# Performance work log

Hardware: AMD Instinct MI355X
Metric: run time of the kernel (lower is better)

Reference implementation:

```python
import jax, jax.numpy as jnp
import numpy as np

EMBED_DIM = 1024
NUM_HEADS = 16
SEQ = 2048
BATCH = 2


def setup_inputs() -> dict:
    key = jax.random.key(0)
    ks = jax.random.split(key, 9)
    E = EMBED_DIM
    gain = 1.0 / np.sqrt(2.0)  # xavier_uniform with gain 1/sqrt(2) (qkv_same_dim)
    limit = gain * np.sqrt(6.0 / (E + E))
    q = jax.random.normal(ks[0], (SEQ, BATCH, E), dtype=jnp.float32)
    k = jax.random.normal(ks[1], (SEQ, BATCH, E), dtype=jnp.float32)
    v = jax.random.normal(ks[2], (SEQ, BATCH, E), dtype=jnp.float32)
    Wq = jax.random.uniform(ks[3], (E, E), jnp.float32, -limit, limit)
    Wk = jax.random.uniform(ks[4], (E, E), jnp.float32, -limit, limit)
    Wv = jax.random.uniform(ks[5], (E, E), jnp.float32, -limit, limit)
    bq = jnp.zeros((E,), jnp.float32)
    bk = jnp.zeros((E,), jnp.float32)
    bv = jnp.zeros((E,), jnp.float32)
    return {"query": q, "key": k, "value": v,
            "Wq": Wq, "bq": bq, "Wk": Wk, "bk": bk, "Wv": Wv, "bv": bv}


def reference(query, key, value, Wq, bq, Wk, bk, Wv, bv):
    # Base Taylor attention path (norm_taylor=True, do_scale=True, has_out=False).
    L, B, E = query.shape
    H = NUM_HEADS
    hd = E // H
    scaling = E ** (-0.5)  # self.scaling = dim**-0.5, dim == embed_dim

    q = (query @ Wq + bq) * scaling          # (L, B, E)
    k = key @ Wk + bk                         # (S, B, E)
    v = value @ Wv + bv                       # (S, B, E)

    def split_heads(x):
        # (T, B, E) -> (B*H, T, hd)
        T = x.shape[0]
        return x.reshape(T, B * H, hd).transpose(1, 0, 2)

    qh, kh, vh = split_heads(q), split_heads(k), split_heads(v)

    # Taylor expansion of exp(qk) to first order: 1 + q.k
    attn = 1.0 + jnp.einsum('bld,bsd->bls', qh, kh)   # (B*H, L, S)
    attn = attn / attn.sum(axis=-1, keepdims=True)    # row-normalize
    out = jnp.einsum('bls,bsd->bld', attn, vh)        # (B*H, L, hd)
    out = out.transpose(1, 0, 2).reshape(L, B, E)     # (L, B, E)
    return out
```

## Files before the change

kernel.cpp:

```cpp
#include <hip/hip_runtime.h>
#include <hip/hip_bf16.h>

#define L_SEQ 2048
#define BATCH 2
#define ROWS 4096
#define E 1024
#define NH 16
#define HD 64

typedef __attribute__((ext_vector_type(4))) float f32x4;
typedef __attribute__((ext_vector_type(8))) __bf16 bf16x8;

#define SWZ(byt) ((byt) ^ ((((byt) >> 7) & 7) << 4))

__device__ __forceinline__ void gload16(const void* g, void* l) {
    __builtin_amdgcn_global_load_lds((const __attribute__((address_space(1))) void*)g,
                                     (__attribute__((address_space(3))) void*)l,
                                     16, 0, 0);
}

__global__ __launch_bounds__(256) void convert_x(const float* __restrict__ q,
                                                 const float* __restrict__ k,
                                                 const float* __restrict__ v,
                                                 __bf16* __restrict__ Xb) {
    const int z = blockIdx.y;
    const float* src = (z == 0) ? q : ((z == 1) ? k : v);
    __bf16* dst = Xb + (size_t)z * ROWS * E;
    const size_t i = ((size_t)blockIdx.x * 256 + threadIdx.x) * 8;
    const float4 a = *(const float4*)(src + i);
    const float4 b = *(const float4*)(src + i + 4);
    bf16x8 o;
    o[0] = (__bf16)a.x; o[1] = (__bf16)a.y; o[2] = (__bf16)a.z; o[3] = (__bf16)a.w;
    o[4] = (__bf16)b.x; o[5] = (__bf16)b.y; o[6] = (__bf16)b.z; o[7] = (__bf16)b.w;
    *(bf16x8*)(dst + i) = o;
}

__global__ __launch_bounds__(256) void transpose_w(const float* __restrict__ Wq,
                                                   const float* __restrict__ Wk,
                                                   const float* __restrict__ Wv,
                                                   __bf16* __restrict__ Wt) {
    const int z = blockIdx.z;
    const float* W = (z == 0) ? Wq : ((z == 1) ? Wk : Wv);
    __bf16* dst = Wt + (size_t)z * E * E;
    __shared__ __align__(16) float t[64][65];
    const int n0 = blockIdx.x * 64, k0 = blockIdx.y * 64;
    const int r = threadIdx.x >> 2, c4 = threadIdx.x & 3;
#pragma unroll
    for (int j = 0; j < 4; ++j) {
        const float4 vv = *(const float4*)&W[(size_t)(k0 + r) * E + n0 + c4 * 16 + j * 4];
        t[r][c4 * 16 + j * 4 + 0] = vv.x;
        t[r][c4 * 16 + j * 4 + 1] = vv.y;
        t[r][c4 * 16 + j * 4 + 2] = vv.z;
        t[r][c4 * 16 + j * 4 + 3] = vv.w;
    }
    __syncthreads();
    bf16x8 o0, o1;
#pragma unroll
    for (int j = 0; j < 8; ++j) {
        o0[j] = (__bf16)t[c4 * 16 + j][r];
        o1[j] = (__bf16)t[c4 * 16 + 8 + j][r];
    }
    *(bf16x8*)&dst[(size_t)(n0 + r) * E + k0 + c4 * 16] = o0;
    *(bf16x8*)&dst[(size_t)(n0 + r) * E + k0 + c4 * 16 + 8] = o1;
}

__device__ __forceinline__ void stage_ht(const __bf16* __restrict__ gsrc, int row0, int kcol,
                                         char* ldsdst, int wv, int ln) {
#pragma unroll
    for (int r = 0; r < 2; ++r) {
        const int rowg = row0 + r * 64 + wv * 8 + (ln >> 3);
        const int c16 = (ln & 7) ^ (ln >> 3);
        gload16(gsrc + (size_t)rowg * E + kcol + c16 * 8,
                ldsdst + r * 8192 + wv * 1024);
    }
}

__device__ __forceinline__ bf16x8 fragld(const char* base, int row, int kk, int kg) {
    return *(const bf16x8*)(base + row * 128 + ((((kk << 2) | kg) ^ (row & 7)) << 4));
}

#define PH_SYNC_BEGIN  __builtin_amdgcn_s_barrier(); \
                       asm volatile("s_waitcnt lgkmcnt(0)" ::: "memory"); \
                       __builtin_amdgcn_sched_barrier(0); \
                       __builtin_amdgcn_s_setprio(1);
#define PH_SYNC_END    __builtin_amdgcn_s_setprio(0); \
                       __builtin_amdgcn_s_barrier();

__global__ __launch_bounds__(512, 2) void gemm_qkv(const __bf16* __restrict__ Xb,
                                                   const __bf16* __restrict__ Wt,
                                                   const float* __restrict__ bq,
                                                   const float* __restrict__ bk,
                                                   const float* __restrict__ bv,
                                                   __bf16* __restrict__ Cb) {
    extern __shared__ __align__(16) char smem[];
    const int z = blockIdx.z;
    const __bf16* A = Xb + (size_t)z * ROWS * E;
    const __bf16* B = Wt + (size_t)z * E * E;
    __bf16* C = Cb + (size_t)z * ROWS * E;
    const float* bias = (z == 0) ? bq : ((z == 1) ? bk : bv);
    const float alpha = (z == 0) ? 0.03125f : 1.0f;
    const int m0 = blockIdx.y * 256, n0 = blockIdx.x * 256;
    const int tid = threadIdx.x, ln = tid & 63, wv = tid >> 6;
    const int lr = ln & 15, kg = ln >> 4;
    const int wm = (wv & 3) * 64, wn = (wv >> 2) * 128;
    char* LA0 = smem;            char* LA1 = smem + 32768;
    char* LB0 = smem + 65536;    char* LB1 = smem + 98304;

    stage_ht(A, m0 + 0,   0,  LA0 + 0,     wv, ln);
    stage_ht(A, m0 + 128, 0,  LA0 + 16384, wv, ln);
    stage_ht(B, n0 + 0,   0,  LB0 + 0,     wv, ln);
    stage_ht(B, n0 + 128, 0,  LB0 + 16384, wv, ln);
    stage_ht(A, m0 + 0,   64, LA1 + 0,     wv, ln);
    stage_ht(A, m0 + 128, 64, LA1 + 16384, wv, ln);
    asm volatile("s_waitcnt vmcnt(4)" ::: "memory");
    __builtin_amdgcn_s_barrier();

    f32x4 acc[4][8] = {};
    bf16x8 Af[4][2], Bf[2][2];

#define LOAD_B(nb) \
    _Pragma("unroll") for (int nn = 0; nn < 2; ++nn) \
    _Pragma("unroll") for (int kk = 0; kk < 2; ++kk) \
        Bf[nn][kk] = fragld(cB, wn + ((nb) + nn) * 16 + lr, kk, kg);
#define QUAD(q) \
    _Pragma("unroll") for (int m = 0; m < 4; ++m) \
    _Pragma("unroll") for (int nn = 0; nn < 2; ++nn) \
    _Pragma("unroll") for (int kk = 0; kk < 2; ++kk) \
        acc[m][2 * (q) + nn] = __builtin_amdgcn_mfma_f32_16x16x32_bf16(Af[m][kk], Bf[nn][kk], acc[m][2 * (q) + nn], 0, 0, 0);

    for (int T = 0; T < 16; ++T) {
        const char* cA = (T & 1) ? LA1 : LA0;
        const char* cB = (T & 1) ? LB1 : LB0;
        char* nB = (T & 1) ? LB0 : LB1;
        char* nA = (T & 1) ? LA1 : LA0;
#pragma unroll
        for (int m = 0; m < 4; ++m)
#pragma unroll
            for (int kk = 0; kk < 2; ++kk)
                Af[m][kk] = fragld(cA, wm + m * 16 + lr, kk, kg);
        LOAD_B(0);
        if (T < 15) stage_ht(B, n0 + 0, (T + 1) * 64, nB + 0, wv, ln);
        PH_SYNC_BEGIN; QUAD(0); PH_SYNC_END;
        LOAD_B(2);
        if (T < 15) stage_ht(B, n0 + 128, (T + 1) * 64, nB + 16384, wv, ln);
        PH_SYNC_BEGIN; QUAD(1); PH_SYNC_END;
        LOAD_B(4);
        if (T < 14) stage_ht(A, m0 + 0, (T + 2) * 64, nA + 0, wv, ln);
        PH_SYNC_BEGIN; QUAD(2); PH_SYNC_END;
        LOAD_B(6);
        if (T < 14) stage_ht(A, m0 + 128, (T + 2) * 64, nA + 16384, wv, ln);
        PH_SYNC_BEGIN; QUAD(3);
        __builtin_amdgcn_s_setprio(0);
        if (T < 14)       { asm volatile("s_waitcnt vmcnt(4)" ::: "memory"); }
        else if (T == 14) { asm volatile("s_waitcnt vmcnt(0)" ::: "memory"); }
        __builtin_amdgcn_s_barrier();
    }
#undef LOAD_B
#undef QUAD

#pragma unroll
    for (int m = 0; m < 4; ++m) {
        const int rbase = m0 + wm + m * 16 + kg * 4;
#pragma unroll
        for (int n = 0; n < 8; ++n) {
            const int col = n0 + wn + n * 16 + lr;
            const float bcol = bias[col];
#pragma unroll
            for (int rr = 0; rr < 4; ++rr)
                C[(size_t)(rbase + rr) * E + col] = (__bf16)((acc[m][n][rr] + bcol) * alpha);
        }
    }
}

__global__ __launch_bounds__(256) void reduce_kv(const __bf16* __restrict__ Kb,
                                                 const __bf16* __restrict__ Vb,
                                                 float* __restrict__ Mpart,
                                                 float* __restrict__ ksumP,
                                                 float* __restrict__ vsumP) {
    const int bh = blockIdx.x, b = bh >> 4, h = bh & 15;
    const int ts = blockIdx.y;
    const int t0 = ts * 128;
    __shared__ __align__(16) __bf16 sK[128 * 64];
    __shared__ __align__(16) __bf16 sV[128 * 64];
    __shared__ float red_k[4][64];
    __shared__ float red_v[4][64];
    const int tid = threadIdx.x;
    const int lane = tid & 63, wave = tid >> 6;
    const int lr = lane & 15, kg = lane >> 4;

    float vk[8] = {}, vv[8] = {};
    const int d0 = (tid & 7) * 8;
#pragma unroll
    for (int i = 0; i < 4; ++i) {
        const int t = i * 32 + (tid >> 3);
        const size_t g = (size_t)((t0 + t) * 2 + b) * E + h * 64 + d0;
        const bf16x8 kv = *(const bf16x8*)&Kb[g];
        const bf16x8 vvv = *(const bf16x8*)&Vb[g];
        const int lo = (t * 128 + d0 * 2) ^ (wave << 5);
        *(bf16x8*)((char*)sK + lo) = kv;
        *(bf16x8*)((char*)sV + lo) = vvv;
#pragma unroll
        for (int j = 0; j < 8; ++j) { vk[j] += (float)kv[j]; vv[j] += (float)vvv[j]; }
    }
#pragma unroll
    for (int m = 8; m <= 32; m <<= 1)
#pragma unroll
        for (int j = 0; j < 8; ++j) {
            vk[j] += __shfl_xor(vk[j], m, 64);
            vv[j] += __shfl_xor(vv[j], m, 64);
        }
    if (lane < 8)
#pragma unroll
        for (int j = 0; j < 8; ++j) {
            red_k[wave][lane * 8 + j] = vk[j];
            red_v[wave][lane * 8 + j] = vv[j];
        }
    __syncthreads();

    f32x4 acc[4] = {};
#pragma unroll
    for (int kt = 0; kt < 4; ++kt) {
        const int tb = kt * 32;
        bf16x8 afr, bfr[4];
        const char* pv = (const char*)sV + (((tb + kg * 8) * 128 + (wave * 16 + lr) * 2) ^ (kg << 5));
#pragma unroll
        for (int j = 0; j < 8; ++j) afr[j] = *(const __bf16*)(pv + j * 128);
#pragma unroll
        for (int ni = 0; ni < 4; ++ni) {
            const char* pk = (const char*)sK + (((tb + kg * 8) * 128 + (ni * 16 + lr) * 2) ^ (kg << 5));
#pragma unroll
            for (int j = 0; j < 8; ++j) bfr[ni][j] = *(const __bf16*)(pk + j * 128);
        }
#pragma unroll
        for (int ni = 0; ni < 4; ++ni)
            acc[ni] = __builtin_amdgcn_mfma_f32_16x16x32_bf16(afr, bfr[ni], acc[ni], 0, 0, 0);
    }

    float* Mp = Mpart + ((size_t)bh * 16 + ts) * 4096;
#pragma unroll
    for (int ni = 0; ni < 4; ++ni)
#pragma unroll
        for (int rr = 0; rr < 4; ++rr)
            Mp[(wave * 16 + kg * 4 + rr) * 64 + ni * 16 + lr] = acc[ni][rr];
    if (tid < 64)
        ksumP[(bh * 16 + ts) * 64 + tid] = red_k[0][tid] + red_k[1][tid] + red_k[2][tid] + red_k[3][tid];
    else if (tid < 128) {
        const int d = tid - 64;
        vsumP[(bh * 16 + ts) * 64 + d] = red_v[0][d] + red_v[1][d] + red_v[2][d] + red_v[3][d];
    }
}

__global__ __launch_bounds__(256) void combine_m(const float* __restrict__ Mpart,
                                                 const float* __restrict__ ksumP,
                                                 const float* __restrict__ vsumP,
                                                 float* __restrict__ Mt,
                                                 float* __restrict__ ksum,
                                                 float* __restrict__ vsum) {
    const int blk = blockIdx.x, tid = threadIdx.x;
    if (blk < 256) {
        const int e2 = (blk * 256 + tid) * 2;
        const int bh = e2 >> 12, r = e2 & 4095;
        const float* src = Mpart + (size_t)bh * 16 * 4096 + r;
        float s0 = 0.f, s1 = 0.f;
#pragma unroll
        for (int ts = 0; ts < 16; ++ts) {
            s0 += src[ts * 4096];
            s1 += src[ts * 4096 + 1];
        }
        Mt[(size_t)bh * 4096 + r] = s0;
        Mt[(size_t)bh * 4096 + r + 1] = s1;
    } else if (blk < 264) {
        const int idx = (blk - 256) * 256 + tid;
        const int bh = idx >> 6, d = idx & 63;
        float s = 0.f;
#pragma unroll
        for (int ts = 0; ts < 16; ++ts) s += ksumP[bh * 1024 + ts * 64 + d];
        ksum[idx] = s;
    } else {
        const int idx = (blk - 264) * 256 + tid;
        const int bh = idx >> 6, d = idx & 63;
        float s = 0.f;
#pragma unroll
        for (int ts = 0; ts < 16; ++ts) s += vsumP[bh * 1024 + ts * 64 + d];
        vsum[idx] = s;
    }
}

__global__ __launch_bounds__(256) void taylor_out(const __bf16* __restrict__ Qb,
                                                  const float* __restrict__ Mt,
                                                  const float* __restrict__ ksum,
                                                  const float* __restrict__ vsum,
                                                  float* __restrict__ out) {
    const int b = blockIdx.y;
    const int lblk = blockIdx.x * 16;
    const int tid = threadIdx.x, lane = tid & 63, wave = tid >> 6;
    const int lr = lane & 15, kg = lane >> 4;
    __shared__ __align__(16) __bf16 sM[4][4096];
    for (int hh = 0; hh < 4; ++hh) {
        __syncthreads();
#pragma unroll
        for (int i = 0; i < 8; ++i) {
            const int idx = i * 256 + tid;
            const int hseg = idx >> 9, rem = idx & 511;
            const float* src = &Mt[(size_t)(b * 16 + hseg * 4 + hh) * 4096 + rem * 8];
            const float4 mA = *(const float4*)src;
            const float4 mB = *(const float4*)(src + 4);
            bf16x8 o;
            o[0] = (__bf16)mA.x; o[1] = (__bf16)mA.y; o[2] = (__bf16)mA.z; o[3] = (__bf16)mA.w;
            o[4] = (__bf16)mB.x; o[5] = (__bf16)mB.y; o[6] = (__bf16)mB.z; o[7] = (__bf16)mB.w;
            *(bf16x8*)((char*)&sM[hseg][0] + SWZ(rem * 16)) = o;
        }
        __syncthreads();
        const int h = wave * 4 + hh;
        const int bh = b * 16 + h;
        const int rA = (lblk + lr) * 2 + b;
        const bf16x8 a0 = *(const bf16x8*)&Qb[(size_t)rA * E + h * 64 + kg * 8];
        const bf16x8 a1 = *(const bf16x8*)&Qb[(size_t)rA * E + h * 64 + 32 + kg * 8];
        float p = 0.f;
        const float* ks = &ksum[bh * 64];
#pragma unroll
        for (int j = 0; j < 8; ++j)
            p += (float)a0[j] * ks[kg * 8 + j] + (float)a1[j] * ks[32 + kg * 8 + j];
        p += __shfl_xor(p, 16, 64);
        p += __shfl_xor(p, 32, 64);
        const float Z = 2048.0f + p;
        f32x4 acc[4] = {};
#pragma unroll
        for (int ni = 0; ni < 4; ++ni) {
            const int byt0 = (ni * 16 + lr) * 128 + kg * 16;
            const bf16x8 b0 = *(const bf16x8*)((const char*)&sM[wave][0] + SWZ(byt0));
            const bf16x8 b1 = *(const bf16x8*)((const char*)&sM[wave][0] + SWZ(byt0 + 64));
            acc[ni] = __builtin_amdgcn_mfma_f32_16x16x32_bf16(a0, b0, acc[ni], 0, 0, 0);
            acc[ni] = __builtin_amdgcn_mfma_f32_16x16x32_bf16(a1, b1, acc[ni], 0, 0, 0);
        }
        float invZ[4];
#pragma unroll
        for (int rr = 0; rr < 4; ++rr) invZ[rr] = 1.0f / __shfl(Z, kg * 4 + rr, 64);
        const float* vs = &vsum[bh * 64];
#pragma unroll
        for (int ni = 0; ni < 4; ++ni)
#pragma unroll
            for (int rr = 0; rr < 4; ++rr) {
                const int l_out = lblk + kg * 4 + rr;
                out[(size_t)(l_out * 2 + b) * E + h * 64 + ni * 16 + lr] =
                    (vs[ni * 16 + lr] + acc[ni][rr]) * invZ[rr];
            }
    }
}

extern "C" void kernel_launch(void* const* d_in, const int* in_sizes, int n_in,
                              void* d_out, int out_size, void* d_ws, size_t ws_size,
                              hipStream_t stream) {
    const float* q  = (const float*)d_in[0];
    const float* k  = (const float*)d_in[1];
    const float* v  = (const float*)d_in[2];
    const float* Wq = (const float*)d_in[3];
    const float* bq = (const float*)d_in[4];
    const float* Wk = (const float*)d_in[5];
    const float* bk = (const float*)d_in[6];
    const float* Wv = (const float*)d_in[7];
    const float* bv = (const float*)d_in[8];
    float* out = (float*)d_out;
    char* w = (char*)d_ws;
    __bf16* Xb = (__bf16*)(w);
    __bf16* Wt = (__bf16*)(w + 25165824);
    __bf16* Cb = (__bf16*)(w + 31457280);
    float* Mt   = (float*)(w + 56623104);
    float* ksum = (float*)(w + 57147392);
    float* vsum = (float*)(w + 57155584);
    float* Mpart = (float*)(w);
    float* ksumP = (float*)(w + 8388608);
    float* vsumP = (float*)(w + 8519680);

    hipFuncSetAttribute((const void*)gemm_qkv,
                        hipFuncAttributeMaxDynamicSharedMemorySize, 131072);
    convert_x<<<dim3(2048, 3), 256, 0, stream>>>(q, k, v, Xb);
    transpose_w<<<dim3(16, 16, 3), 256, 0, stream>>>(Wq, Wk, Wv, Wt);
    gemm_qkv<<<dim3(4, 16, 3), 512, 131072, stream>>>(Xb, Wt, bq, bk, bv, Cb);
    reduce_kv<<<dim3(32, 16), 256, 0, stream>>>(Cb + (size_t)ROWS * E,
                                                Cb + 2 * (size_t)ROWS * E, Mpart, ksumP, vsumP);
    combine_m<<<272, 256, 0, stream>>>(Mpart, ksumP, vsumP, Mt, ksum, vsum);
    taylor_out<<<dim3(128, 2), 256, 0, stream>>>(Cb, Mt, ksum, vsum, out);
}
```

Baseline: 77.44 us.

## Shrink QKV GEMM tiles to 128x128 and merge prep kernels

Measured after the change: 82.27 us. 1.06x slower.

```diff
diff --git a/kernel.cpp b/kernel.cpp
--- a/kernel.cpp
+++ b/kernel.cpp
@@ -19,31 +19,32 @@
                                      16, 0, 0);
 }
 
-__global__ __launch_bounds__(256) void convert_x(const float* __restrict__ q,
-                                                 const float* __restrict__ k,
-                                                 const float* __restrict__ v,
-                                                 __bf16* __restrict__ Xb) {
+__global__ __launch_bounds__(256) void prep(const float* __restrict__ q,
+                                            const float* __restrict__ k,
+                                            const float* __restrict__ v,
+                                            const float* __restrict__ Wq,
+                                            const float* __restrict__ Wk,
+                                            const float* __restrict__ Wv,
+                                            __bf16* __restrict__ Xb,
+                                            __bf16* __restrict__ Wt) {
     const int z = blockIdx.y;
-    const float* src = (z == 0) ? q : ((z == 1) ? k : v);
-    __bf16* dst = Xb + (size_t)z * ROWS * E;
-    const size_t i = ((size_t)blockIdx.x * 256 + threadIdx.x) * 8;
-    const float4 a = *(const float4*)(src + i);
-    const float4 b = *(const float4*)(src + i + 4);
-    bf16x8 o;
-    o[0] = (__bf16)a.x; o[1] = (__bf16)a.y; o[2] = (__bf16)a.z; o[3] = (__bf16)a.w;
-    o[4] = (__bf16)b.x; o[5] = (__bf16)b.y; o[6] = (__bf16)b.z; o[7] = (__bf16)b.w;
-    *(bf16x8*)(dst + i) = o;
-}
-
-__global__ __launch_bounds__(256) void transpose_w(const float* __restrict__ Wq,
-                                                   const float* __restrict__ Wk,
-                                                   const float* __restrict__ Wv,
-                                                   __bf16* __restrict__ Wt) {
-    const int z = blockIdx.z;
+    if (blockIdx.x < 2048) {
+        const float* src = (z == 0) ? q : ((z == 1) ? k : v);
+        __bf16* dst = Xb + (size_t)z * ROWS * E;
+        const size_t i = ((size_t)blockIdx.x * 256 + threadIdx.x) * 8;
+        const float4 a = *(const float4*)(src + i);
+        const float4 b = *(const float4*)(src + i + 4);
+        bf16x8 o;
+        o[0] = (__bf16)a.x; o[1] = (__bf16)a.y; o[2] = (__bf16)a.z; o[3] = (__bf16)a.w;
+        o[4] = (__bf16)b.x; o[5] = (__bf16)b.y; o[6] = (__bf16)b.z; o[7] = (__bf16)b.w;
+        *(bf16x8*)(dst + i) = o;
+        return;
+    }
     const float* W = (z == 0) ? Wq : ((z == 1) ? Wk : Wv);
     __bf16* dst = Wt + (size_t)z * E * E;
     __shared__ __align__(16) float t[64][65];
-    const int n0 = blockIdx.x * 64, k0 = blockIdx.y * 64;
+    const int tt = blockIdx.x - 2048;
+    const int n0 = (tt & 15) * 64, k0 = (tt >> 4) * 64;
     const int r = threadIdx.x >> 2, c4 = threadIdx.x & 3;
 #pragma unroll
     for (int j = 0; j < 4; ++j) {
@@ -64,14 +65,14 @@
     *(bf16x8*)&dst[(size_t)(n0 + r) * E + k0 + c4 * 16 + 8] = o1;
 }
 
-__device__ __forceinline__ void stage_ht(const __bf16* __restrict__ gsrc, int row0, int kcol,
-                                         char* ldsdst, int wv, int ln) {
-#pragma unroll
-    for (int r = 0; r < 2; ++r) {
-        const int rowg = row0 + r * 64 + wv * 8 + (ln >> 3);
+__device__ __forceinline__ void stage_tile(const __bf16* __restrict__ gsrc, int row0, int kcol,
+                                           char* ldsdst, int wv, int ln) {
+#pragma unroll
+    for (int r = 0; r < 4; ++r) {
+        const int rowg = row0 + r * 32 + wv * 8 + (ln >> 3);
         const int c16 = (ln & 7) ^ (ln >> 3);
         gload16(gsrc + (size_t)rowg * E + kcol + c16 * 8,
-                ldsdst + r * 8192 + wv * 1024);
+                ldsdst + r * 4096 + wv * 1024);
     }
 }
 
@@ -81,41 +82,37 @@
 
 #define PH_SYNC_BEGIN  __builtin_amdgcn_s_barrier(); \
                        asm volatile("s_waitcnt lgkmcnt(0)" ::: "memory"); \
-                       __builtin_amdgcn_sched_barrier(0); \
                        __builtin_amdgcn_s_setprio(1);
 #define PH_SYNC_END    __builtin_amdgcn_s_setprio(0); \
                        __builtin_amdgcn_s_barrier();
 
-__global__ __launch_bounds__(512, 2) void gemm_qkv(const __bf16* __restrict__ Xb,
+__global__ __launch_bounds__(256, 2) void gemm_qkv(const __bf16* __restrict__ Xb,
                                                    const __bf16* __restrict__ Wt,
                                                    const float* __restrict__ bq,
                                                    const float* __restrict__ bk,
                                                    const float* __restrict__ bv,
                                                    __bf16* __restrict__ Cb) {
-    extern __shared__ __align__(16) char smem[];
+    __shared__ __align__(16) char smem[65536];
     const int z = blockIdx.z;
     const __bf16* A = Xb + (size_t)z * ROWS * E;
     const __bf16* B = Wt + (size_t)z * E * E;
     __bf16* C = Cb + (size_t)z * ROWS * E;
     const float* bias = (z == 0) ? bq : ((z == 1) ? bk : bv);
     const float alpha = (z == 0) ? 0.03125f : 1.0f;
-    const int m0 = blockIdx.y * 256, n0 = blockIdx.x * 256;
+    const int m0 = blockIdx.y * 128, n0 = blockIdx.x * 128;
     const int tid = threadIdx.x, ln = tid & 63, wv = tid >> 6;
     const int lr = ln & 15, kg = ln >> 4;
-    const int wm = (wv & 3) * 64, wn = (wv >> 2) * 128;
-    char* LA0 = smem;            char* LA1 = smem + 32768;
-    char* LB0 = smem + 65536;    char* LB1 = smem + 98304;
-
-    stage_ht(A, m0 + 0,   0,  LA0 + 0,     wv, ln);
-    stage_ht(A, m0 + 128, 0,  LA0 + 16384, wv, ln);
-    stage_ht(B, n0 + 0,   0,  LB0 + 0,     wv, ln);
-    stage_ht(B, n0 + 128, 0,  LB0 + 16384, wv, ln);
-    stage_ht(A, m0 + 0,   64, LA1 + 0,     wv, ln);
-    stage_ht(A, m0 + 128, 64, LA1 + 16384, wv, ln);
+    const int wm = (wv & 1) * 64, wn = (wv >> 1) * 64;
+    char* LA0 = smem;            char* LA1 = smem + 16384;
+    char* LB0 = smem + 32768;    char* LB1 = smem + 49152;
+
+    stage_tile(A, m0, 0,  LA0, wv, ln);
+    stage_tile(B, n0, 0,  LB0, wv, ln);
+    stage_tile(A, m0, 64, LA1, wv, ln);
     asm volatile("s_waitcnt vmcnt(4)" ::: "memory");
     __builtin_amdgcn_s_barrier();
 
-    f32x4 acc[4][8] = {};
+    f32x4 acc[4][4] = {};
     bf16x8 Af[4][2], Bf[2][2];
 
 #define LOAD_B(nb) \
@@ -139,17 +136,11 @@
             for (int kk = 0; kk < 2; ++kk)
                 Af[m][kk] = fragld(cA, wm + m * 16 + lr, kk, kg);
         LOAD_B(0);
-        if (T < 15) stage_ht(B, n0 + 0, (T + 1) * 64, nB + 0, wv, ln);
+        if (T < 15) stage_tile(B, n0, (T + 1) * 64, nB, wv, ln);
         PH_SYNC_BEGIN; QUAD(0); PH_SYNC_END;
         LOAD_B(2);
-        if (T < 15) stage_ht(B, n0 + 128, (T + 1) * 64, nB + 16384, wv, ln);
-        PH_SYNC_BEGIN; QUAD(1); PH_SYNC_END;
-        LOAD_B(4);
-        if (T < 14) stage_ht(A, m0 + 0, (T + 2) * 64, nA + 0, wv, ln);
-        PH_SYNC_BEGIN; QUAD(2); PH_SYNC_END;
-        LOAD_B(6);
-        if (T < 14) stage_ht(A, m0 + 128, (T + 2) * 64, nA + 16384, wv, ln);
-        PH_SYNC_BEGIN; QUAD(3);
+        if (T < 14) stage_tile(A, m0, (T + 2) * 64, nA, wv, ln);
+        PH_SYNC_BEGIN; QUAD(1);
         __builtin_amdgcn_s_setprio(0);
         if (T < 14)       { asm volatile("s_waitcnt vmcnt(4)" ::: "memory"); }
         else if (T == 14) { asm volatile("s_waitcnt vmcnt(0)" ::: "memory"); }
@@ -162,7 +153,7 @@
     for (int m = 0; m < 4; ++m) {
         const int rbase = m0 + wm + m * 16 + kg * 4;
 #pragma unroll
-        for (int n = 0; n < 8; ++n) {
+        for (int n = 0; n < 4; ++n) {
             const int col = n0 + wn + n * 16 + lr;
             const float bcol = bias[col];
 #pragma unroll
@@ -372,11 +363,8 @@
     float* ksumP = (float*)(w + 8388608);
     float* vsumP = (float*)(w + 8519680);
 
-    hipFuncSetAttribute((const void*)gemm_qkv,
-                        hipFuncAttributeMaxDynamicSharedMemorySize, 131072);
-    convert_x<<<dim3(2048, 3), 256, 0, stream>>>(q, k, v, Xb);
-    transpose_w<<<dim3(16, 16, 3), 256, 0, stream>>>(Wq, Wk, Wv, Wt);
-    gemm_qkv<<<dim3(4, 16, 3), 512, 131072, stream>>>(Xb, Wt, bq, bk, bv, Cb);
+    prep<<<dim3(2304, 3), 256, 0, stream>>>(q, k, v, Wq, Wk, Wv, Xb, Wt);
+    gemm_qkv<<<dim3(8, 32, 3), 256, 0, stream>>>(Xb, Wt, bq, bk, bv, Cb);
     reduce_kv<<<dim3(32, 16), 256, 0, stream>>>(Cb + (size_t)ROWS * E,
                                                 Cb + 2 * (size_t)ROWS * E, Mpart, ksumP, vsumP);
     combine_m<<<272, 256, 0, stream>>>(Mpart, ksumP, vsumP, Mt, ksum, vsum);
```
